# Optimization experiments

Measured on AMD Instinct MI355X. Metric: run time of the kernel, lower is better.

## Reference

```python
import jax, jax.numpy as jnp
import numpy as np

TAU = 0.5
EPS = 1e-8  # torch CosineSimilarity default eps


def _cosine_logits(a, b, tau):
    # a: [N, D], b: [N, D] -> [N, N] cosine similarity / tau
    a_n = a / jnp.maximum(jnp.linalg.norm(a, axis=-1, keepdims=True), EPS)
    b_n = b / jnp.maximum(jnp.linalg.norm(b, axis=-1, keepdims=True), EPS)
    return jnp.einsum('nd,md->nm', a_n, b_n) / tau


def _ce_diag(logits):
    # cross-entropy with targets = arange(N), mean over rows
    logp = jax.nn.log_softmax(logits, axis=-1)
    return -jnp.mean(jnp.diagonal(logp))


def setup_inputs() -> dict:
    key = jax.random.key(0)
    kx, ky = jax.random.split(key)
    N, D = 8192, 512
    x = jax.random.normal(kx, (N, D), dtype=jnp.float32)
    y = jax.random.normal(ky, (N, D), dtype=jnp.float32)
    return {"x": x, "y": y}


def reference(x, y):
    sim_xy = _cosine_logits(x, y, TAU)  # [N, N]
    sim_yx = _cosine_logits(y, x, TAU)  # [N, N]
    return (_ce_diag(sim_xy) + _ce_diag(sim_yx)) / 2.0
```

## Files before the change

### kernel.cpp

```cpp
#include <hip/hip_runtime.h>
#include <hip/hip_bf16.h>
#include <stdint.h>


#define NROWS 8192
#define DDIM  512
#define TAU_INV 2.0f

typedef __bf16 bf16x8 __attribute__((ext_vector_type(8)));
typedef __bf16 bf16x4 __attribute__((ext_vector_type(4)));
typedef float  f32x4  __attribute__((ext_vector_type(4)));
typedef __attribute__((address_space(3))) const __bf16 lds_cbf16;

#define DSR(d, b, o) asm volatile("ds_read_b128 %0, %1 offset:%c2" \
                                  : "=v"(d) : "v"(b), "i"(o))

__device__ __forceinline__ void gload(const __bf16* src, __bf16* dst) {
  __builtin_amdgcn_global_load_lds((__attribute__((address_space(1))) void*)src,
      (__attribute__((address_space(3))) void*)dst, 16, 0, 0);
}

__global__ __launch_bounds__(256) void normalize_kernel(
    const float* __restrict__ x, const float* __restrict__ y,
    __bf16* __restrict__ xn, __bf16* __restrict__ yn,
    float* __restrict__ rowsum, float* __restrict__ colsum,
    float* __restrict__ out) {
  const int idx = blockIdx.x * 256 + (int)threadIdx.x;
  if (idx < NROWS) { rowsum[idx] = 0.0f; colsum[idx] = 0.0f; }
  if (idx == 0) out[0] = 0.0f;

  const int wave = threadIdx.x >> 6;
  const int lane = threadIdx.x & 63;
  const int row  = blockIdx.x * 4 + wave;
  const float* src;
  __bf16* dst;
  if (row < NROWS) { src = x + (size_t)row * DDIM;           dst = xn + (size_t)row * DDIM; }
  else             { src = y + (size_t)(row - NROWS) * DDIM; dst = yn + (size_t)(row - NROWS) * DDIM; }

  const float4* s4 = (const float4*)src;
  float4 v0 = s4[lane];
  float4 v1 = s4[lane + 64];
  float ss = v0.x*v0.x + v0.y*v0.y + v0.z*v0.z + v0.w*v0.w
           + v1.x*v1.x + v1.y*v1.y + v1.z*v1.z + v1.w*v1.w;
  #pragma unroll
  for (int off = 1; off < 64; off <<= 1) ss += __shfl_xor(ss, off);
  const float rn = 1.0f / fmaxf(sqrtf(ss), 1e-8f);

  bf16x4 o0, o1;
  o0[0]=(__bf16)(v0.x*rn); o0[1]=(__bf16)(v0.y*rn); o0[2]=(__bf16)(v0.z*rn); o0[3]=(__bf16)(v0.w*rn);
  o1[0]=(__bf16)(v1.x*rn); o1[1]=(__bf16)(v1.y*rn); o1[2]=(__bf16)(v1.z*rn); o1[3]=(__bf16)(v1.w*rn);
  *(bf16x4*)(dst + 4*lane)       = o0;
  *(bf16x4*)(dst + 256 + 4*lane) = o1;
}

template<int T>
__device__ __forceinline__ void body(
    const __bf16* __restrict__ PA, const __bf16* __restrict__ PB,
    __bf16* __restrict__ sm, int tid,
    uint32_t arB0, uint32_t arB1, uint32_t brB0, uint32_t brB1,
    bf16x8 (&aB)[2][8], bf16x8 (&bB)[2][8], f32x4 (&acc)[4][4]) {
  if constexpr (T <= 6) {
    constexpr int S = T + 1, bufS = S & 1;
    const __bf16* pa = PA + S * 64;
    gload(pa,          sm + bufS*8192 + tid*8);
    gload(pa + 32768,  sm + bufS*8192 + 4096 + tid*8);
    const __bf16* pb = PB + S * 64;
    gload(pb,          sm + 16384 + bufS*16384 + tid*8);
    gload(pb + 32768,  sm + 16384 + bufS*16384 + 4096  + tid*8);
    gload(pb + 65536,  sm + 16384 + bufS*16384 + 8192  + tid*8);
    gload(pb + 98304,  sm + 16384 + bufS*16384 + 12288 + tid*8);
  }
  {
    constexpr int bk = T & 1, AO = bk * 16384, BO = bk * 32768;
    DSR(aB[bk][0], arB0, AO + 0);    DSR(aB[bk][1], arB1, AO + 0);
    DSR(aB[bk][2], arB0, AO + 2048); DSR(aB[bk][3], arB1, AO + 2048);
    DSR(aB[bk][4], arB0, AO + 4096); DSR(aB[bk][5], arB1, AO + 4096);
    DSR(aB[bk][6], arB0, AO + 6144); DSR(aB[bk][7], arB1, AO + 6144);
    DSR(bB[bk][0], brB0, BO + 0);    DSR(bB[bk][1], brB1, BO + 0);
    DSR(bB[bk][2], brB0, BO + 2048); DSR(bB[bk][3], brB1, BO + 2048);
    DSR(bB[bk][4], brB0, BO + 4096); DSR(bB[bk][5], brB1, BO + 4096);
    DSR(bB[bk][6], brB0, BO + 6144); DSR(bB[bk][7], brB1, BO + 6144);
  }
  __builtin_amdgcn_sched_barrier(0);
  if constexpr (T >= 1) {
    constexpr int pb2 = (T - 1) & 1;
    __builtin_amdgcn_s_setprio(1);
    #pragma unroll
    for (int mi = 0; mi < 4; ++mi)
      #pragma unroll
      for (int ni = 0; ni < 4; ++ni) {
        acc[mi][ni] = __builtin_amdgcn_mfma_f32_16x16x32_bf16(aB[pb2][mi*2+0], bB[pb2][ni*2+0], acc[mi][ni], 0,0,0);
        acc[mi][ni] = __builtin_amdgcn_mfma_f32_16x16x32_bf16(aB[pb2][mi*2+1], bB[pb2][ni*2+1], acc[mi][ni], 0,0,0);
      }
    __builtin_amdgcn_s_setprio(0);
  }
  asm volatile("s_waitcnt vmcnt(0) lgkmcnt(0)" ::: "memory");
  __builtin_amdgcn_s_barrier();
  __builtin_amdgcn_sched_barrier(0);
}

__global__ __launch_bounds__(512, 2) void gemm_exp_kernel(
    const __bf16* __restrict__ Xn, const __bf16* __restrict__ Yn,
    float* __restrict__ rowsum, float* __restrict__ colsum,
    float* __restrict__ diag) {
  __shared__ __bf16 sm[49152];

  const int tid  = threadIdx.x;
  const int lane = tid & 63;
  const int w    = tid >> 6;
  const int wr   = w >> 2;
  const int wc   = w & 3;

  const int id  = blockIdx.x;
  const int swz = (id & 7) * 256 + (id >> 3);
  const int bi  = swz & 63;
  const int bj  = swz >> 6;
  const int Ar = bi * 128;
  const int Br = bj * 256;

  const int l15 = lane & 15;
  const int g   = lane >> 4;
  const int sw  = g ^ (l15 & 7);

  const int r0  = tid >> 3;
  const int sc0 = (tid & 7) ^ (r0 & 7);
  const __bf16* PA = Xn + (size_t)(Ar + r0) * DDIM + sc0 * 8;
  const __bf16* PB = Yn + (size_t)(Br + r0) * DDIM + sc0 * 8;

  const uint32_t ldsb = (uint32_t)(uintptr_t)(lds_cbf16*)sm;
  const uint32_t arB0 = ldsb + (uint32_t)((wr*64 + l15)*128 + sw*16);
  const uint32_t arB1 = arB0 ^ 64u;
  const uint32_t brB0 = ldsb + 32768u + (uint32_t)((wc*64 + l15)*128 + sw*16);
  const uint32_t brB1 = brB0 ^ 64u;

  bf16x8 aB[2][8], bB[2][8];
  f32x4 acc[4][4] = {};

  gload(PA,          sm + tid*8);
  gload(PA + 32768,  sm + 4096 + tid*8);
  gload(PB,          sm + 16384 + tid*8);
  gload(PB + 32768,  sm + 16384 + 4096  + tid*8);
  gload(PB + 65536,  sm + 16384 + 8192  + tid*8);
  gload(PB + 98304,  sm + 16384 + 12288 + tid*8);
  asm volatile("s_waitcnt vmcnt(0)" ::: "memory");
  __builtin_amdgcn_s_barrier();
  __builtin_amdgcn_sched_barrier(0);

  body<0>(PA, PB, sm, tid, arB0, arB1, brB0, brB1, aB, bB, acc);
  body<1>(PA, PB, sm, tid, arB0, arB1, brB0, brB1, aB, bB, acc);
  body<2>(PA, PB, sm, tid, arB0, arB1, brB0, brB1, aB, bB, acc);
  body<3>(PA, PB, sm, tid, arB0, arB1, brB0, brB1, aB, bB, acc);
  body<4>(PA, PB, sm, tid, arB0, arB1, brB0, brB1, aB, bB, acc);
  body<5>(PA, PB, sm, tid, arB0, arB1, brB0, brB1, aB, bB, acc);
  body<6>(PA, PB, sm, tid, arB0, arB1, brB0, brB1, aB, bB, acc);
  body<7>(PA, PB, sm, tid, arB0, arB1, brB0, brB1, aB, bB, acc);
  __builtin_amdgcn_s_setprio(1);
  #pragma unroll
  for (int mi = 0; mi < 4; ++mi)
    #pragma unroll
    for (int ni = 0; ni < 4; ++ni) {
      acc[mi][ni] = __builtin_amdgcn_mfma_f32_16x16x32_bf16(aB[1][mi*2+0], bB[1][ni*2+0], acc[mi][ni], 0,0,0);
      acc[mi][ni] = __builtin_amdgcn_mfma_f32_16x16x32_bf16(aB[1][mi*2+1], bB[1][ni*2+1], acc[mi][ni], 0,0,0);
    }
  __builtin_amdgcn_s_setprio(0);

  int RL[4], CL[4];
  #pragma unroll
  for (int m = 0; m < 4; ++m) RL[m] = wr*64 + m*16;
  #pragma unroll
  for (int n = 0; n < 4; ++n) CL[n] = wc*64 + n*16;

  if ((bi >> 1) == bj) {
    #pragma unroll
    for (int m = 0; m < 4; ++m)
      #pragma unroll
      for (int n = 0; n < 4; ++n)
        #pragma unroll
        for (int r = 0; r < 4; ++r) {
          const int grow = Ar + RL[m] + g*4 + r, gcol = Br + CL[n] + l15;
          if (grow == gcol) diag[grow] = TAU_INV * acc[m][n][r];
        }
  }

  #pragma unroll
  for (int m = 0; m < 4; ++m)
    #pragma unroll
    for (int n = 0; n < 4; ++n)
      #pragma unroll
      for (int r = 0; r < 4; ++r)
        acc[m][n][r] = __expf(TAU_INV * acc[m][n][r]);

  #pragma unroll
  for (int m = 0; m < 4; ++m) {
    #pragma unroll
    for (int r = 0; r < 4; ++r) {
      float v = acc[m][0][r] + acc[m][1][r] + acc[m][2][r] + acc[m][3][r];
      v += __shfl_xor(v, 1); v += __shfl_xor(v, 2);
      v += __shfl_xor(v, 4); v += __shfl_xor(v, 8);
      if (l15 == 0) atomicAdd(&rowsum[Ar + RL[m] + g*4 + r], v);
    }
  }
  #pragma unroll
  for (int n = 0; n < 4; ++n) {
    float v = 0.0f;
    #pragma unroll
    for (int m = 0; m < 4; ++m)
      #pragma unroll
      for (int r = 0; r < 4; ++r)
        v += acc[m][n][r];
    v += __shfl_xor(v, 16); v += __shfl_xor(v, 32);
    if (lane < 16) atomicAdd(&colsum[Br + CL[n] + l15], v);
  }
}

__global__ __launch_bounds__(256) void finalize_kernel(
    const float* __restrict__ rowsum, const float* __restrict__ colsum,
    const float* __restrict__ diag, float* __restrict__ out) {
  const int i = blockIdx.x * 256 + (int)threadIdx.x;
  float s = 0.5f * (logf(rowsum[i]) + logf(colsum[i])) - diag[i];
  #pragma unroll
  for (int off = 1; off < 64; off <<= 1) s += __shfl_xor(s, off);
  if ((threadIdx.x & 63) == 0) atomicAdd(out, s * (1.0f / NROWS));
}

extern "C" void kernel_launch(void* const* d_in, const int* in_sizes, int n_in,
                              void* d_out, int out_size, void* d_ws, size_t ws_size,
                              hipStream_t stream) {
  const float* x = (const float*)d_in[0];
  const float* y = (const float*)d_in[1];
  float* out = (float*)d_out;

  char* ws = (char*)d_ws;
  __bf16* Xn = (__bf16*)ws;
  __bf16* Yn = Xn + (size_t)NROWS * DDIM;
  float* rowsum = (float*)(ws + 2 * (size_t)NROWS * DDIM * sizeof(__bf16));
  float* colsum = rowsum + NROWS;
  float* diag   = colsum + NROWS;

  normalize_kernel<<<(2 * NROWS) / 4, 256, 0, stream>>>(x, y, Xn, Yn, rowsum, colsum, out);
  gemm_exp_kernel<<<2048, 512, 0, stream>>>(Xn, Yn, rowsum, colsum, diag);
  finalize_kernel<<<32, 256, 0, stream>>>(rowsum, colsum, diag, out);
}
```

Baseline: 182.6 us.

## Triple-buffer LDS tiles with prefetch distance two in GEMM mainloop

The GEMM K-loop moves from double to triple buffering in shared memory and issues global-to-LDS loads two stages ahead. The per-iteration wait becomes a partial vmcnt, so one stage of loads can stay in flight across the barrier instead of draining every step. This is meant to hide global memory latency behind the MFMA work. In exchange LDS use rises to 144 KB per block, which may limit occupancy at the requested two blocks per CU.

```diff
diff --git a/kernel.cpp b/kernel.cpp
--- a/kernel.cpp
+++ b/kernel.cpp
@@ -53,33 +53,39 @@
   *(bf16x4*)(dst + 256 + 4*lane) = o1;
 }
 
+template<int S>
+__device__ __forceinline__ void stage(
+    const __bf16* __restrict__ PA, const __bf16* __restrict__ PB,
+    __bf16* __restrict__ sm, int tid) {
+  constexpr int buf = S % 3;
+  const __bf16* pa = PA + S * 64;
+  gload(pa,          sm + buf*8192 + tid*8);
+  gload(pa + 32768,  sm + buf*8192 + 4096 + tid*8);
+  const __bf16* pb = PB + S * 64;
+  gload(pb,          sm + 24576 + buf*16384 + tid*8);
+  gload(pb + 32768,  sm + 24576 + buf*16384 + 4096  + tid*8);
+  gload(pb + 65536,  sm + 24576 + buf*16384 + 8192  + tid*8);
+  gload(pb + 98304,  sm + 24576 + buf*16384 + 12288 + tid*8);
+}
+
 template<int T>
 __device__ __forceinline__ void body(
     const __bf16* __restrict__ PA, const __bf16* __restrict__ PB,
     __bf16* __restrict__ sm, int tid,
-    uint32_t arB0, uint32_t arB1, uint32_t brB0, uint32_t brB1,
+    const uint32_t (&aB0)[3], const uint32_t (&aB1)[3],
+    const uint32_t (&bB0)[3], const uint32_t (&bB1)[3],
     bf16x8 (&aB)[2][8], bf16x8 (&bB)[2][8], f32x4 (&acc)[4][4]) {
-  if constexpr (T <= 6) {
-    constexpr int S = T + 1, bufS = S & 1;
-    const __bf16* pa = PA + S * 64;
-    gload(pa,          sm + bufS*8192 + tid*8);
-    gload(pa + 32768,  sm + bufS*8192 + 4096 + tid*8);
-    const __bf16* pb = PB + S * 64;
-    gload(pb,          sm + 16384 + bufS*16384 + tid*8);
-    gload(pb + 32768,  sm + 16384 + bufS*16384 + 4096  + tid*8);
-    gload(pb + 65536,  sm + 16384 + bufS*16384 + 8192  + tid*8);
-    gload(pb + 98304,  sm + 16384 + bufS*16384 + 12288 + tid*8);
-  }
+  if constexpr (T <= 5) stage<T + 2>(PA, PB, sm, tid);
   {
-    constexpr int bk = T & 1, AO = bk * 16384, BO = bk * 32768;
-    DSR(aB[bk][0], arB0, AO + 0);    DSR(aB[bk][1], arB1, AO + 0);
-    DSR(aB[bk][2], arB0, AO + 2048); DSR(aB[bk][3], arB1, AO + 2048);
-    DSR(aB[bk][4], arB0, AO + 4096); DSR(aB[bk][5], arB1, AO + 4096);
-    DSR(aB[bk][6], arB0, AO + 6144); DSR(aB[bk][7], arB1, AO + 6144);
-    DSR(bB[bk][0], brB0, BO + 0);    DSR(bB[bk][1], brB1, BO + 0);
-    DSR(bB[bk][2], brB0, BO + 2048); DSR(bB[bk][3], brB1, BO + 2048);
-    DSR(bB[bk][4], brB0, BO + 4096); DSR(bB[bk][5], brB1, BO + 4096);
-    DSR(bB[bk][6], brB0, BO + 6144); DSR(bB[bk][7], brB1, BO + 6144);
+    constexpr int rb = T % 3, bk = T & 1;
+    DSR(aB[bk][0], aB0[rb], 0);    DSR(aB[bk][1], aB1[rb], 0);
+    DSR(aB[bk][2], aB0[rb], 2048); DSR(aB[bk][3], aB1[rb], 2048);
+    DSR(aB[bk][4], aB0[rb], 4096); DSR(aB[bk][5], aB1[rb], 4096);
+    DSR(aB[bk][6], aB0[rb], 6144); DSR(aB[bk][7], aB1[rb], 6144);
+    DSR(bB[bk][0], bB0[rb], 0);    DSR(bB[bk][1], bB1[rb], 0);
+    DSR(bB[bk][2], bB0[rb], 2048); DSR(bB[bk][3], bB1[rb], 2048);
+    DSR(bB[bk][4], bB0[rb], 4096); DSR(bB[bk][5], bB1[rb], 4096);
+    DSR(bB[bk][6], bB0[rb], 6144); DSR(bB[bk][7], bB1[rb], 6144);
   }
   __builtin_amdgcn_sched_barrier(0);
   if constexpr (T >= 1) {
@@ -94,8 +100,10 @@
       }
     __builtin_amdgcn_s_setprio(0);
   }
-  asm volatile("s_waitcnt vmcnt(0) lgkmcnt(0)" ::: "memory");
-  __builtin_amdgcn_s_barrier();
+  if constexpr (T <= 5)      asm volatile("s_waitcnt vmcnt(6) lgkmcnt(0)" ::: "memory");
+  else if constexpr (T == 6) asm volatile("s_waitcnt vmcnt(0) lgkmcnt(0)" ::: "memory");
+  else                       asm volatile("s_waitcnt lgkmcnt(0)" ::: "memory");
+  if constexpr (T < 7) __builtin_amdgcn_s_barrier();
   __builtin_amdgcn_sched_barrier(0);
 }
 
@@ -103,7 +111,7 @@
     const __bf16* __restrict__ Xn, const __bf16* __restrict__ Yn,
     float* __restrict__ rowsum, float* __restrict__ colsum,
     float* __restrict__ diag) {
-  __shared__ __bf16 sm[49152];
+  __shared__ __bf16 sm[73728];
 
   const int tid  = threadIdx.x;
   const int lane = tid & 63;
@@ -128,32 +136,32 @@
   const __bf16* PB = Yn + (size_t)(Br + r0) * DDIM + sc0 * 8;
 
   const uint32_t ldsb = (uint32_t)(uintptr_t)(lds_cbf16*)sm;
-  const uint32_t arB0 = ldsb + (uint32_t)((wr*64 + l15)*128 + sw*16);
-  const uint32_t arB1 = arB0 ^ 64u;
-  const uint32_t brB0 = ldsb + 32768u + (uint32_t)((wc*64 + l15)*128 + sw*16);
-  const uint32_t brB1 = brB0 ^ 64u;
+  uint32_t aB0r[3], aB1r[3], bB0r[3], bB1r[3];
+  #pragma unroll
+  for (int b = 0; b < 3; ++b) {
+    aB0r[b] = ldsb + b*16384u + (uint32_t)((wr*64 + l15)*128 + sw*16);
+    aB1r[b] = aB0r[b] ^ 64u;
+    bB0r[b] = ldsb + 49152u + b*32768u + (uint32_t)((wc*64 + l15)*128 + sw*16);
+    bB1r[b] = bB0r[b] ^ 64u;
+  }
 
   bf16x8 aB[2][8], bB[2][8];
   f32x4 acc[4][4] = {};
 
-  gload(PA,          sm + tid*8);
-  gload(PA + 32768,  sm + 4096 + tid*8);
-  gload(PB,          sm + 16384 + tid*8);
-  gload(PB + 32768,  sm + 16384 + 4096  + tid*8);
-  gload(PB + 65536,  sm + 16384 + 8192  + tid*8);
-  gload(PB + 98304,  sm + 16384 + 12288 + tid*8);
-  asm volatile("s_waitcnt vmcnt(0)" ::: "memory");
+  stage<0>(PA, PB, sm, tid);
+  stage<1>(PA, PB, sm, tid);
+  asm volatile("s_waitcnt vmcnt(6)" ::: "memory");
   __builtin_amdgcn_s_barrier();
   __builtin_amdgcn_sched_barrier(0);
 
-  body<0>(PA, PB, sm, tid, arB0, arB1, brB0, brB1, aB, bB, acc);
-  body<1>(PA, PB, sm, tid, arB0, arB1, brB0, brB1, aB, bB, acc);
-  body<2>(PA, PB, sm, tid, arB0, arB1, brB0, brB1, aB, bB, acc);
-  body<3>(PA, PB, sm, tid, arB0, arB1, brB0, brB1, aB, bB, acc);
-  body<4>(PA, PB, sm, tid, arB0, arB1, brB0, brB1, aB, bB, acc);
-  body<5>(PA, PB, sm, tid, arB0, arB1, brB0, brB1, aB, bB, acc);
-  body<6>(PA, PB, sm, tid, arB0, arB1, brB0, brB1, aB, bB, acc);
-  body<7>(PA, PB, sm, tid, arB0, arB1, brB0, brB1, aB, bB, acc);
+  body<0>(PA, PB, sm, tid, aB0r, aB1r, bB0r, bB1r, aB, bB, acc);
+  body<1>(PA, PB, sm, tid, aB0r, aB1r, bB0r, bB1r, aB, bB, acc);
+  body<2>(PA, PB, sm, tid, aB0r, aB1r, bB0r, bB1r, aB, bB, acc);
+  body<3>(PA, PB, sm, tid, aB0r, aB1r, bB0r, bB1r, aB, bB, acc);
+  body<4>(PA, PB, sm, tid, aB0r, aB1r, bB0r, bB1r, aB, bB, acc);
+  body<5>(PA, PB, sm, tid, aB0r, aB1r, bB0r, bB1r, aB, bB, acc);
+  body<6>(PA, PB, sm, tid, aB0r, aB1r, bB0r, bB1r, aB, bB, acc);
+  body<7>(PA, PB, sm, tid, aB0r, aB1r, bB0r, bB1r, aB, bB, acc);
   __builtin_amdgcn_s_setprio(1);
   #pragma unroll
   for (int mi = 0; mi < 4; ++mi)
```

After: 178.6 us. 2.2% less time.
